# Kernel tuning notes

Hardware: AMD Instinct MI355X
Metric: run time of the kernel (lower is better)

Reference implementation:

```python
import jax, jax.numpy as jnp
import numpy as np
import math

B, S, D, H = 2, 2048, 1024, 16
HD = D // H  # head_dim = 64


def setup_inputs() -> dict:
    rng = jax.random.key(0)
    ks = jax.random.split(rng, 11)
    std = 1.0 / math.sqrt(D)
    inp = {
        "query": jax.random.normal(ks[0], (B, S, D), dtype=jnp.float32),
        "key": jax.random.normal(ks[1], (B, S, D), dtype=jnp.float32),
        "value": jax.random.normal(ks[2], (B, S, D), dtype=jnp.float32),
        # causal mask: True = masked (ignored), matching masked_fill semantics
        "mask": jnp.triu(jnp.ones((S, S), dtype=bool), k=1),
        "wq": jax.random.normal(ks[3], (D, D), dtype=jnp.float32) * std,
        "bq": jnp.zeros((D,), dtype=jnp.float32),
        "wk": jax.random.normal(ks[4], (D, D), dtype=jnp.float32) * std,
        "bk": jnp.zeros((D,), dtype=jnp.float32),
        "wv": jax.random.normal(ks[5], (D, D), dtype=jnp.float32) * std,
        "bv": jnp.zeros((D,), dtype=jnp.float32),
        "wo": jax.random.normal(ks[6], (D, D), dtype=jnp.float32) * std,
        "bo": jnp.zeros((D,), dtype=jnp.float32),
    }
    return inp


def reference(query, key, value, mask, wq, bq, wk, bk, wv, bv, wo, bo):
    # Linear projections (torch Linear: x @ W.T + b)
    q = jnp.einsum('bsd,ed->bse', query, wq) + bq
    k = jnp.einsum('bsd,ed->bse', key, wk) + bk
    v = jnp.einsum('bsd,ed->bse', value, wv) + bv
    # split heads: (B, S, D) -> (B, H, S, HD)
    q = q.reshape(B, S, H, HD).transpose(0, 2, 1, 3)
    k = k.reshape(B, S, H, HD).transpose(0, 2, 1, 3)
    v = v.reshape(B, S, H, HD).transpose(0, 2, 1, 3)
    # naive attention: materialize full (B, H, Sq, Sk) scores
    scores = jnp.einsum('bhqd,bhkd->bhqk', q, k) / jnp.sqrt(jnp.float32(HD))
    scores = jnp.where(mask[None, None, :, :], -jnp.inf, scores)
    attn = jax.nn.softmax(scores, axis=-1)
    out = jnp.einsum('bhqk,bhkd->bhqd', attn, v)
    out = out.transpose(0, 2, 1, 3).reshape(B, S, D)
    return jnp.einsum('bsd,ed->bse', out, wo) + bo
```

## Files before the change

kernel.cpp:

```cpp
#include <hip/hip_runtime.h>
#include <stdint.h>

#define B_ 2
#define S_ 2048
#define D_ 1024
#define H_ 16
#define HD_ 64
#define M_TOT (B_*S_)
#define NSPL 3

typedef __bf16 bf16;
typedef bf16 bf16x8 __attribute__((ext_vector_type(8)));
typedef float f32x4 __attribute__((ext_vector_type(4)));
typedef float f32x16 __attribute__((ext_vector_type(16)));
typedef unsigned int u32;
typedef unsigned int u32x4v __attribute__((ext_vector_type(4)));

__device__ __forceinline__ void gload_lds16(const void* g, void* l) {
    __builtin_amdgcn_global_load_lds((const __attribute__((address_space(1))) void*)g,
                                     (__attribute__((address_space(3))) void*)l, 16, 0, 0);
}

__device__ __forceinline__ u32 cvtpk_bf16(float lo, float hi) {
    u32 d;
    asm("v_cvt_pk_bf16_f32 %0, %1, %2" : "=v"(d) : "v"(lo), "v"(hi));
    return d;
}

__global__ __launch_bounds__(256) void cvt_kernel(
    const float* __restrict__ q, const float* __restrict__ k, const float* __restrict__ v,
    const float* __restrict__ wq, const float* __restrict__ wk,
    const float* __restrict__ wv, const float* __restrict__ wo,
    bf16* __restrict__ xq, bf16* __restrict__ xk, bf16* __restrict__ xv,
    bf16* __restrict__ wqb, bf16* __restrict__ wkb, bf16* __restrict__ wvb, bf16* __restrict__ wob)
{
    const float* src; bf16* dst; int n;
    switch (blockIdx.y) {
        case 0: src=q;  dst=xq;  n=M_TOT*D_; break;
        case 1: src=k;  dst=xk;  n=M_TOT*D_; break;
        case 2: src=v;  dst=xv;  n=M_TOT*D_; break;
        case 3: src=wq; dst=wqb; n=D_*D_;    break;
        case 4: src=wk; dst=wkb; n=D_*D_;    break;
        case 5: src=wv; dst=wvb; n=D_*D_;    break;
        default: src=wo; dst=wob; n=D_*D_;   break;
    }
    int i = (blockIdx.x*blockDim.x + threadIdx.x)*8;
    if (i >= n) return;
    const f32x4* s4 = (const f32x4*)(src + i);
    f32x4 a = s4[0], b = s4[1];
    bf16x8 o;
    #pragma unroll
    for (int j = 0; j < 4; ++j) { o[j] = (bf16)a[j]; o[j+4] = (bf16)b[j]; }
    *(bf16x8*)(dst + i) = o;
}

__device__ __forceinline__ void gemm_mainloop(const bf16* __restrict__ A, const bf16* __restrict__ Wt,
                                              int brow, int bcol, bf16* As, bf16* Bs,
                                              f32x4 (&acc)[4][4])
{
    const int tid = threadIdx.x;
    const int l = tid & 63, w = tid >> 6;
    const int wr = w >> 1, wc = w & 1;
    const int lr = l & 15, lq = l >> 4;

    for (int k0 = 0; k0 < D_; k0 += 32) {
        #pragma unroll
        for (int i = 0; i < 2; ++i) {
            int id = i*256 + tid;
            int row = id >> 2, c8 = (id & 3) << 3;
            gload_lds16(A  + (size_t)(brow + row)*D_ + k0 + c8, As + id*8);
            gload_lds16(Wt + (size_t)(bcol + row)*D_ + k0 + c8, Bs + id*8);
        }
        __syncthreads();
        bf16x8 af[4], bf[4];
        #pragma unroll
        for (int m = 0; m < 4; ++m)
            af[m] = *(const bf16x8*)&As[(wr*64 + m*16 + lr)*32 + lq*8];
        #pragma unroll
        for (int n = 0; n < 4; ++n)
            bf[n] = *(const bf16x8*)&Bs[(wc*64 + n*16 + lr)*32 + lq*8];
        #pragma unroll
        for (int m = 0; m < 4; ++m)
            #pragma unroll
            for (int n = 0; n < 4; ++n)
                acc[m][n] = __builtin_amdgcn_mfma_f32_16x16x32_bf16(af[m], bf[n], acc[m][n], 0, 0, 0);
        __syncthreads();
    }
}

__global__ __launch_bounds__(256) void gemm_qkv(
    const bf16* __restrict__ xq, const bf16* __restrict__ xk, const bf16* __restrict__ xv,
    const bf16* __restrict__ wqb, const bf16* __restrict__ wkb, const bf16* __restrict__ wvb,
    const float* __restrict__ bq, const float* __restrict__ bk, const float* __restrict__ bv,
    bf16* __restrict__ Qf, bf16* __restrict__ Kf, bf16* __restrict__ Vf)
{
    __shared__ __align__(16) bf16 As[128*32];
    __shared__ __align__(16) bf16 Bs[128*32];
    const int z = blockIdx.z;
    const bf16* A  = (z==0) ? xq  : (z==1) ? xk  : xv;
    const bf16* Wt = (z==0) ? wqb : (z==1) ? wkb : wvb;
    const float* bias = (z==0) ? bq : (z==1) ? bk : bv;

    const int brow = (blockIdx.x & 31)*128;
    const int bcol = (blockIdx.x >> 5)*128;

    f32x4 acc[4][4] = {};
    gemm_mainloop(A, Wt, brow, bcol, As, Bs, acc);

    const int tid = threadIdx.x;
    const int l = tid & 63, w = tid >> 6;
    const int wr = w >> 1, wc = w & 1;
    const int lr = l & 15, lq = l >> 4;

    #pragma unroll
    for (int m = 0; m < 4; ++m)
        #pragma unroll
        for (int n = 0; n < 4; ++n) {
            int col = bcol + wc*64 + n*16 + lr;
            float bv_ = bias[col];
            int h = col >> 6, hd = col & 63;
            #pragma unroll
            for (int r = 0; r < 4; ++r) {
                int row = brow + wr*64 + m*16 + lq*4 + r;
                int b = row >> 11, s = row & 2047;
                float val = acc[m][n][r] + bv_;
                if (z == 0) val *= 0.18033688011112042f;
                size_t hbase = ((size_t)b*H_ + h)*S_*HD_;
                if (z < 2) {
                    int chunk = ((s >> 5) << 2) + (hd >> 4);
                    int lane  = (((hd >> 3) & 1) << 5) | (s & 31);
                    bf16* dst = (z==0) ? Qf : Kf;
                    dst[hbase + (size_t)chunk*512 + lane*8 + (hd & 7)] = (bf16)val;
                } else {
                    int chunk = ((s >> 6) << 3) + (((s >> 4) & 3) << 1) + (hd >> 5);
                    int lane  = (((s >> 3) & 1) << 5) | (hd & 31);
                    Vf[hbase + (size_t)chunk*512 + lane*8 + (s & 7)] = (bf16)val;
                }
            }
        }
}

__global__ __launch_bounds__(256) void gemm_out(
    const bf16* __restrict__ Oat, const bf16* __restrict__ wob,
    const float* __restrict__ bo, float* __restrict__ out)
{
    __shared__ __align__(16) bf16 As[128*32];
    __shared__ __align__(16) bf16 Bs[128*32];
    const int brow = (blockIdx.x & 31)*128;
    const int bcol = (blockIdx.x >> 5)*128;

    f32x4 acc[4][4] = {};
    gemm_mainloop(Oat, wob, brow, bcol, As, Bs, acc);

    const int tid = threadIdx.x;
    const int l = tid & 63, w = tid >> 6;
    const int wr = w >> 1, wc = w & 1;
    const int lr = l & 15, lq = l >> 4;

    #pragma unroll
    for (int m = 0; m < 4; ++m)
        #pragma unroll
        for (int n = 0; n < 4; ++n) {
            int col = bcol + wc*64 + n*16 + lr;
            float bv_ = bo[col];
            #pragma unroll
            for (int r = 0; r < 4; ++r) {
                int row = brow + wr*64 + m*16 + lq*4 + r;
                out[(size_t)row*D_ + col] = acc[m][n][r] + bv_;
            }
        }
}

#define ATTN_BODY(CUR, NXT, KT) do {                                                        \
    const int kc0_ = (KT)*64;                                                               \
    const bool last_ = ((KT) == nkt - 1);                                                   \
    const int ktn_ = ((KT) + 1 < te) ? (KT) + 1 : (KT);                                     \
    bf16x8 va0[4], va1[4];                                                                  \
    _Pragma("unroll")                                                                       \
    for (int c = 0; c < 4; ++c) {                                                           \
        va0[c] = *(const bf16x8*)(Vfp + (size_t)((KT)*8 + c*2 + 0)*512 + l8);               \
        va1[c] = *(const bf16x8*)(Vfp + (size_t)((KT)*8 + c*2 + 1)*512 + l8);               \
    }                                                                                       \
    _Pragma("unroll")                                                                       \
    for (int kv2 = 0; kv2 < 2; ++kv2)                                                       \
        _Pragma("unroll")                                                                   \
        for (int dc = 0; dc < 4; ++dc)                                                      \
            NXT[kv2][dc] = *(const bf16x8*)(Kfp + (size_t)((ktn_*2 + kv2)*4 + dc)*512 + l8);\
    f32x16 ct0 = {}, ct1 = {};                                                              \
    __builtin_amdgcn_s_setprio(1);                                                          \
    _Pragma("unroll")                                                                       \
    for (int dc = 0; dc < 4; ++dc)                                                          \
        ct0 = __builtin_amdgcn_mfma_f32_32x32x16_bf16(CUR[0][dc], qb[dc], ct0, 0, 0, 0);    \
    _Pragma("unroll")                                                                       \
    for (int dc = 0; dc < 4; ++dc)                                                          \
        ct1 = __builtin_amdgcn_mfma_f32_32x32x16_bf16(CUR[1][dc], qb[dc], ct1, 0, 0, 0);    \
    __builtin_amdgcn_s_setprio(0);                                                          \
    if (last_) {                                                                            \
        _Pragma("unroll")                                                                   \
        for (int reg = 0; reg < 16; ++reg) {                                                \
            const int rr = (reg & 3) + 8*(reg >> 2) + 4*hi;                                 \
            if (kc0_ + rr > qrow)      ct0[reg] = -1e30f;                                   \
            if (kc0_ + 32 + rr > qrow) ct1[reg] = -1e30f;                                   \
        }                                                                                   \
    }                                                                                       \
    float t8[8];                                                                            \
    _Pragma("unroll")                                                                       \
    for (int i = 0; i < 8; ++i)                                                             \
        t8[i] = fmaxf(fmaxf(ct0[i], ct0[i+8]), fmaxf(ct1[i], ct1[i+8]));                    \
    float t4a = fmaxf(t8[0], t8[4]), t4b = fmaxf(t8[1], t8[5]);                             \
    float t4c = fmaxf(t8[2], t8[6]), t4d = fmaxf(t8[3], t8[7]);                             \
    float vm = fmaxf(fmaxf(t4a, t4b), fmaxf(t4c, t4d));                                     \
    vm = fmaxf(vm, __shfl_xor(vm, 32));                                                     \
    if (!__all(vm <= mrun + 8.f)) {                                                         \
        float nm = fmaxf(mrun, vm);                                                         \
        float al = exp2f(mrun - nm);                                                        \
        _Pragma("unroll")                                                                   \
        for (int i = 0; i < 16; ++i) { ot0[i] *= al; ot1[i] *= al; }                        \
        lrun *= al;                                                                         \
        mrun = nm;                                                                          \
    }                                                                                       \
    _Pragma("unroll")                                                                       \
    for (int i = 0; i < 16; ++i) {                                                          \
        ct0[i] = exp2f(ct0[i] - mrun);                                                      \
        ct1[i] = exp2f(ct1[i] - mrun);                                                      \
    }                                                                                       \
    float s8[8];                                                                            \
    _Pragma("unroll")                                                                       \
    for (int i = 0; i < 8; ++i)                                                             \
        s8[i] = (ct0[i] + ct0[i+8]) + (ct1[i] + ct1[i+8]);                                  \
    float s4a = s8[0]+s8[4], s4b = s8[1]+s8[5], s4c = s8[2]+s8[6], s4d = s8[3]+s8[7];       \
    float ps = (s4a + s4b) + (s4c + s4d);                                                   \
    ps += __shfl_xor(ps, 32);                                                               \
    lrun += ps;                                                                             \
    u32 own0[8], own1[8], oth0[8], oth1[8];                                                 \
    _Pragma("unroll")                                                                       \
    for (int u = 0; u < 8; ++u) {                                                           \
        own0[u] = cvtpk_bf16(ct0[2*u], ct0[2*u+1]);                                         \
        own1[u] = cvtpk_bf16(ct1[2*u], ct1[2*u+1]);                                         \
    }                                                                                       \
    _Pragma("unroll")                                                                       \
    for (int u = 0; u < 8; ++u) {                                                           \
        oth0[u] = __shfl_xor(own0[u], 32);                                                  \
        oth1[u] = __shfl_xor(own1[u], 32);                                                  \
    }                                                                                       \
    __builtin_amdgcn_s_setprio(1);                                                          \
    _Pragma("unroll")                                                                       \
    for (int c = 0; c < 4; ++c) {                                                           \
        const int b0 = 4*(c & 1);                                                           \
        u32 o0, o1, o2, o3, x0, x1, x2, x3;                                                 \
        if ((c >> 1) == 0) {                                                                \
            o0 = own0[b0]; o1 = own0[b0+1]; o2 = own0[b0+2]; o3 = own0[b0+3];               \
            x0 = oth0[b0]; x1 = oth0[b0+1]; x2 = oth0[b0+2]; x3 = oth0[b0+3];               \
        } else {                                                                            \
            o0 = own1[b0]; o1 = own1[b0+1]; o2 = own1[b0+2]; o3 = own1[b0+3];               \
            x0 = oth1[b0]; x1 = oth1[b0+1]; x2 = oth1[b0+2]; x3 = oth1[b0+3];               \
        }                                                                                   \
        u32 w0 = hi ? x2 : o0;                                                              \
        u32 w1 = hi ? x3 : o1;                                                              \
        u32 w2 = hi ? o2 : x0;                                                              \
        u32 w3 = hi ? o3 : x1;                                                              \
        u32x4v pw = { w0, w1, w2, w3 };                                                     \
        bf16x8 pb = __builtin_bit_cast(bf16x8, pw);                                         \
        ot0 = __builtin_amdgcn_mfma_f32_32x32x16_bf16(va0[c], pb, ot0, 0, 0, 0);            \
        ot1 = __builtin_amdgcn_mfma_f32_32x32x16_bf16(va1[c], pb, ot1, 0, 0, 0);            \
    }                                                                                       \
    __builtin_amdgcn_s_setprio(0);                                                          \
} while (0)

__global__ __launch_bounds__(64, 2) void attn_part(
    const bf16* __restrict__ Qf, const bf16* __restrict__ Kf,
    const bf16* __restrict__ Vf, bf16* __restrict__ Opart, float* __restrict__ Mlf)
{
    const int l = threadIdx.x & 63;
    const int l31 = l & 31, hi = l >> 5;
    const int l8 = l*8;

    const int id = (int)blockIdx.x;
    const int xcd = id & 7;
    const int slot = id >> 3;
    const int bh = xcd + 8*(slot/192);
    const int rem = slot % 192;
    const int qt = 63 - rem/3;
    const int part = rem % 3;
    const int q0 = qt*32;
    const int qrow = q0 + l31;
    const int widx = (bh*64 + qt)*NSPL + part;

    const bf16* Qfp = Qf + (size_t)bh*S_*HD_;
    const bf16* Kfp = Kf + (size_t)bh*S_*HD_;
    const bf16* Vfp = Vf + (size_t)bh*S_*HD_;

    const int nkt = q0/64 + 1;
    const int ts = (part*nkt)/NSPL;
    const int te = ((part+1)*nkt)/NSPL;

    bf16x8 qb[4];
    #pragma unroll
    for (int dc = 0; dc < 4; ++dc)
        qb[dc] = *(const bf16x8*)(Qfp + (size_t)(((q0 >> 5) << 2) + dc)*512 + l8);

    f32x16 ot0 = {}, ot1 = {};
    float mrun = -1e30f, lrun = 0.f;

    if (ts < te) {
        bf16x8 ka[2][4], kb[2][4];
        #pragma unroll
        for (int kv2 = 0; kv2 < 2; ++kv2)
            #pragma unroll
            for (int dc = 0; dc < 4; ++dc)
                ka[kv2][dc] = *(const bf16x8*)(Kfp + (size_t)((ts*2 + kv2)*4 + dc)*512 + l8);

        int kt = ts;
        while (kt + 1 < te) {
            ATTN_BODY(ka, kb, kt); ++kt;
            ATTN_BODY(kb, ka, kt); ++kt;
        }
        if (kt < te) {
            ATTN_BODY(ka, kb, kt);
        }
    }

    bf16* Ob = Opart + (size_t)widx*2048;
    #pragma unroll
    for (int rp = 0; rp < 16; ++rp) {
        const int d0 = (rp & 3) + 8*(rp >> 2) + 4*hi;
        Ob[d0*32 + l31]        = (bf16)ot0[rp];
        Ob[(32 + d0)*32 + l31] = (bf16)ot1[rp];
    }
    if (!hi) {
        Mlf[(size_t)widx*64 + l31*2]     = mrun;
        Mlf[(size_t)widx*64 + l31*2 + 1] = lrun;
    }
}

__global__ __launch_bounds__(64) void attn_combine(
    const bf16* __restrict__ Opart, const float* __restrict__ Mlf, bf16* __restrict__ Oat)
{
    const int cb = (int)blockIdx.x;
    const int bh = cb >> 6, qt = cb & 63;
    const int b = bh >> 4, h = bh & 15;
    const int q0 = qt*32;
    const int l = threadIdx.x & 63;
    const int q = l & 31, hi = l >> 5;

    const int wbase = (bh*64 + qt)*NSPL;
    float mm[NSPL], ll[NSPL];
    #pragma unroll
    for (int p = 0; p < NSPL; ++p) {
        mm[p] = Mlf[(size_t)(wbase+p)*64 + q*2];
        ll[p] = Mlf[(size_t)(wbase+p)*64 + q*2 + 1];
    }
    float m = fmaxf(fmaxf(mm[0], mm[1]), mm[2]);
    float f[NSPL];
    float lt = 0.f;
    #pragma unroll
    for (int p = 0; p < NSPL; ++p) { f[p] = exp2f(mm[p] - m); lt += ll[p]*f[p]; }
    const float inv = 1.f / lt;
    #pragma unroll
    for (int p = 0; p < NSPL; ++p) f[p] *= inv;

    char* rowp = (char*)Oat + (((size_t)(b*S_ + q0 + q)*D_ + h*64 + hi*32)*2);

    #pragma unroll
    for (int i = 0; i < 16; ++i) {
        const int d = hi*32 + 2*i;
        float oA = 0.f, oB = 0.f;
        #pragma unroll
        for (int p = 0; p < NSPL; ++p) {
            const bf16* Op = Opart + (size_t)(wbase+p)*2048;
            oA += (float)Op[d*32 + q]*f[p];
            oB += (float)Op[(d+1)*32 + q]*f[p];
        }
        *(u32*)(rowp + 4*i) = cvtpk_bf16(oA, oB);
    }
}

extern "C" void kernel_launch(void* const* d_in, const int* in_sizes, int n_in,
                              void* d_out, int out_size, void* d_ws, size_t ws_size,
                              hipStream_t stream) {
    const float* q  = (const float*)d_in[0];
    const float* k  = (const float*)d_in[1];
    const float* v  = (const float*)d_in[2];
    const float* wq = (const float*)d_in[4];
    const float* bq = (const float*)d_in[5];
    const float* wk = (const float*)d_in[6];
    const float* bk = (const float*)d_in[7];
    const float* wv = (const float*)d_in[8];
    const float* bv = (const float*)d_in[9];
    const float* wo = (const float*)d_in[10];
    const float* bo = (const float*)d_in[11];
    float* out = (float*)d_out;

    char* p = (char*)d_ws;
    const size_t XSZ = (size_t)M_TOT*D_*sizeof(bf16);
    const size_t WSZ = (size_t)D_*D_*sizeof(bf16);
    bf16* xq  = (bf16*)p;
    bf16* xk  = (bf16*)(p + XSZ);
    bf16* xv  = (bf16*)(p + 2*XSZ);
    bf16* wqb = (bf16*)(p + 3*XSZ);
    bf16* wkb = (bf16*)(p + 3*XSZ + WSZ);
    bf16* wvb = (bf16*)(p + 3*XSZ + 2*WSZ);
    bf16* wob = (bf16*)(p + 3*XSZ + 3*WSZ);
    bf16* Qf  = (bf16*)(p + 3*XSZ + 4*WSZ);
    bf16* Kf  = Qf + M_TOT*D_;
    bf16* Vf  = Kf + M_TOT*D_;
    bf16* Oat = Vf + M_TOT*D_;
    bf16*  Opart = (bf16*)p;
    float* Mlf   = (float*)(p + 3*XSZ);

    cvt_kernel<<<dim3(2048, 7), 256, 0, stream>>>(q, k, v, wq, wk, wv, wo,
                                                  xq, xk, xv, wqb, wkb, wvb, wob);
    gemm_qkv<<<dim3(256, 1, 3), 256, 0, stream>>>(xq, xk, xv, wqb, wkb, wvb,
                                                  bq, bk, bv, Qf, Kf, Vf);
    attn_part<<<32*64*NSPL, 64, 0, stream>>>(Qf, Kf, Vf, Opart, Mlf);
    attn_combine<<<2048, 64, 0, stream>>>(Opart, Mlf, Oat);
    gemm_out<<<dim3(256), 256, 0, stream>>>(Oat, wob, bo, out);
}
```

Measured before the change: 130.4 us.

## Fuse fp32-to-bf16 conversion into GEMM LDS loads and drop conversion kernel

Removes the separate conversion kernel and has the QKV and output GEMMs load fp32 inputs and weights directly into LDS with an XOR swizzle, converting to bf16 when fragments are read. This avoids a full extra read/write pass over activations and weights plus one launch. In exchange, GEMM tiles move twice the bytes through global memory and LDS, and every fragment read repeats the conversion, raising shared memory use and possibly lowering occupancy.

```diff
diff --git a/kernel.cpp b/kernel.cpp
--- a/kernel.cpp
+++ b/kernel.cpp
@@ -27,36 +27,18 @@
     return d;
 }
 
-__global__ __launch_bounds__(256) void cvt_kernel(
-    const float* __restrict__ q, const float* __restrict__ k, const float* __restrict__ v,
-    const float* __restrict__ wq, const float* __restrict__ wk,
-    const float* __restrict__ wv, const float* __restrict__ wo,
-    bf16* __restrict__ xq, bf16* __restrict__ xk, bf16* __restrict__ xv,
-    bf16* __restrict__ wqb, bf16* __restrict__ wkb, bf16* __restrict__ wvb, bf16* __restrict__ wob)
-{
-    const float* src; bf16* dst; int n;
-    switch (blockIdx.y) {
-        case 0: src=q;  dst=xq;  n=M_TOT*D_; break;
-        case 1: src=k;  dst=xk;  n=M_TOT*D_; break;
-        case 2: src=v;  dst=xv;  n=M_TOT*D_; break;
-        case 3: src=wq; dst=wqb; n=D_*D_;    break;
-        case 4: src=wk; dst=wkb; n=D_*D_;    break;
-        case 5: src=wv; dst=wvb; n=D_*D_;    break;
-        default: src=wo; dst=wob; n=D_*D_;   break;
-    }
-    int i = (blockIdx.x*blockDim.x + threadIdx.x)*8;
-    if (i >= n) return;
-    const f32x4* s4 = (const f32x4*)(src + i);
-    f32x4 a = s4[0], b = s4[1];
-    bf16x8 o;
-    #pragma unroll
-    for (int j = 0; j < 4; ++j) { o[j] = (bf16)a[j]; o[j+4] = (bf16)b[j]; }
-    *(bf16x8*)(dst + i) = o;
-}
-
-__device__ __forceinline__ void gemm_mainloop(const bf16* __restrict__ A, const bf16* __restrict__ Wt,
-                                              int brow, int bcol, bf16* As, bf16* Bs,
-                                              f32x4 (&acc)[4][4])
+__device__ __forceinline__ bf16x8 cvt8(f32x4 a, f32x4 b) {
+    u32x4v r;
+    r[0] = cvtpk_bf16(a[0], a[1]);
+    r[1] = cvtpk_bf16(a[2], a[3]);
+    r[2] = cvtpk_bf16(b[0], b[1]);
+    r[3] = cvtpk_bf16(b[2], b[3]);
+    return __builtin_bit_cast(bf16x8, r);
+}
+
+__device__ __forceinline__ void gemm_mainloop_f32(const float* __restrict__ A, const float* __restrict__ Wt,
+                                                  int brow, int bcol, float* As, float* Bs,
+                                                  f32x4 (&acc)[4][4])
 {
     const int tid = threadIdx.x;
     const int l = tid & 63, w = tid >> 6;
@@ -65,20 +47,29 @@
 
     for (int k0 = 0; k0 < D_; k0 += 32) {
         #pragma unroll
-        for (int i = 0; i < 2; ++i) {
+        for (int i = 0; i < 4; ++i) {
             int id = i*256 + tid;
-            int row = id >> 2, c8 = (id & 3) << 3;
-            gload_lds16(A  + (size_t)(brow + row)*D_ + k0 + c8, As + id*8);
-            gload_lds16(Wt + (size_t)(bcol + row)*D_ + k0 + c8, Bs + id*8);
+            int row = id >> 3, c16 = id & 7;
+            int sc = (c16 ^ (row & 7)) << 2;
+            gload_lds16(A  + (size_t)(brow + row)*D_ + k0 + sc, (char*)As + id*16);
+            gload_lds16(Wt + (size_t)(bcol + row)*D_ + k0 + sc, (char*)Bs + id*16);
         }
         __syncthreads();
         bf16x8 af[4], bf[4];
         #pragma unroll
-        for (int m = 0; m < 4; ++m)
-            af[m] = *(const bf16x8*)&As[(wr*64 + m*16 + lr)*32 + lq*8];
-        #pragma unroll
-        for (int n = 0; n < 4; ++n)
-            bf[n] = *(const bf16x8*)&Bs[(wc*64 + n*16 + lr)*32 + lq*8];
+        for (int m = 0; m < 4; ++m) {
+            int row = wr*64 + m*16 + lr, r7 = row & 7;
+            f32x4 a0 = *(const f32x4*)(As + row*32 + (((lq*2    ) ^ r7) << 2));
+            f32x4 a1 = *(const f32x4*)(As + row*32 + (((lq*2 + 1) ^ r7) << 2));
+            af[m] = cvt8(a0, a1);
+        }
+        #pragma unroll
+        for (int n = 0; n < 4; ++n) {
+            int row = wc*64 + n*16 + lr, r7 = row & 7;
+            f32x4 b0 = *(const f32x4*)(Bs + row*32 + (((lq*2    ) ^ r7) << 2));
+            f32x4 b1 = *(const f32x4*)(Bs + row*32 + (((lq*2 + 1) ^ r7) << 2));
+            bf[n] = cvt8(b0, b1);
+        }
         #pragma unroll
         for (int m = 0; m < 4; ++m)
             #pragma unroll
@@ -89,23 +80,23 @@
 }
 
 __global__ __launch_bounds__(256) void gemm_qkv(
-    const bf16* __restrict__ xq, const bf16* __restrict__ xk, const bf16* __restrict__ xv,
-    const bf16* __restrict__ wqb, const bf16* __restrict__ wkb, const bf16* __restrict__ wvb,
+    const float* __restrict__ xq, const float* __restrict__ xk, const float* __restrict__ xv,
+    const float* __restrict__ wqf, const float* __restrict__ wkf, const float* __restrict__ wvf,
     const float* __restrict__ bq, const float* __restrict__ bk, const float* __restrict__ bv,
     bf16* __restrict__ Qf, bf16* __restrict__ Kf, bf16* __restrict__ Vf)
 {
-    __shared__ __align__(16) bf16 As[128*32];
-    __shared__ __align__(16) bf16 Bs[128*32];
+    __shared__ __align__(16) float As[128*32];
+    __shared__ __align__(16) float Bs[128*32];
     const int z = blockIdx.z;
-    const bf16* A  = (z==0) ? xq  : (z==1) ? xk  : xv;
-    const bf16* Wt = (z==0) ? wqb : (z==1) ? wkb : wvb;
+    const float* A  = (z==0) ? xq  : (z==1) ? xk  : xv;
+    const float* Wt = (z==0) ? wqf : (z==1) ? wkf : wvf;
     const float* bias = (z==0) ? bq : (z==1) ? bk : bv;
 
     const int brow = (blockIdx.x & 31)*128;
     const int bcol = (blockIdx.x >> 5)*128;
 
     f32x4 acc[4][4] = {};
-    gemm_mainloop(A, Wt, brow, bcol, As, Bs, acc);
+    gemm_mainloop_f32(A, Wt, brow, bcol, As, Bs, acc);
 
     const int tid = threadIdx.x;
     const int l = tid & 63, w = tid >> 6;
@@ -141,21 +132,54 @@
 }
 
 __global__ __launch_bounds__(256) void gemm_out(
-    const bf16* __restrict__ Oat, const bf16* __restrict__ wob,
+    const bf16* __restrict__ Oat, const float* __restrict__ wof,
     const float* __restrict__ bo, float* __restrict__ out)
 {
-    __shared__ __align__(16) bf16 As[128*32];
-    __shared__ __align__(16) bf16 Bs[128*32];
+    __shared__ __align__(16) bf16  As[128*32];
+    __shared__ __align__(16) float Bs[128*32];
     const int brow = (blockIdx.x & 31)*128;
     const int bcol = (blockIdx.x >> 5)*128;
-
-    f32x4 acc[4][4] = {};
-    gemm_mainloop(Oat, wob, brow, bcol, As, Bs, acc);
 
     const int tid = threadIdx.x;
     const int l = tid & 63, w = tid >> 6;
     const int wr = w >> 1, wc = w & 1;
     const int lr = l & 15, lq = l >> 4;
+
+    f32x4 acc[4][4] = {};
+
+    for (int k0 = 0; k0 < D_; k0 += 32) {
+        #pragma unroll
+        for (int i = 0; i < 2; ++i) {
+            int id = i*256 + tid;
+            int row = id >> 2, c8 = (id & 3) << 3;
+            gload_lds16(Oat + (size_t)(brow + row)*D_ + k0 + c8, (char*)As + id*16);
+        }
+        #pragma unroll
+        for (int i = 0; i < 4; ++i) {
+            int id = i*256 + tid;
+            int row = id >> 3, c16 = id & 7;
+            int sc = (c16 ^ (row & 7)) << 2;
+            gload_lds16(wof + (size_t)(bcol + row)*D_ + k0 + sc, (char*)Bs + id*16);
+        }
+        __syncthreads();
+        bf16x8 af[4], bf[4];
+        #pragma unroll
+        for (int m = 0; m < 4; ++m)
+            af[m] = *(const bf16x8*)&As[(wr*64 + m*16 + lr)*32 + lq*8];
+        #pragma unroll
+        for (int n = 0; n < 4; ++n) {
+            int row = wc*64 + n*16 + lr, r7 = row & 7;
+            f32x4 b0 = *(const f32x4*)(Bs + row*32 + (((lq*2    ) ^ r7) << 2));
+            f32x4 b1 = *(const f32x4*)(Bs + row*32 + (((lq*2 + 1) ^ r7) << 2));
+            bf[n] = cvt8(b0, b1);
+        }
+        #pragma unroll
+        for (int m = 0; m < 4; ++m)
+            #pragma unroll
+            for (int n = 0; n < 4; ++n)
+                acc[m][n] = __builtin_amdgcn_mfma_f32_16x16x32_bf16(af[m], bf[n], acc[m][n], 0, 0, 0);
+        __syncthreads();
+    }
 
     #pragma unroll
     for (int m = 0; m < 4; ++m)
@@ -393,26 +417,16 @@
 
     char* p = (char*)d_ws;
     const size_t XSZ = (size_t)M_TOT*D_*sizeof(bf16);
-    const size_t WSZ = (size_t)D_*D_*sizeof(bf16);
-    bf16* xq  = (bf16*)p;
-    bf16* xk  = (bf16*)(p + XSZ);
-    bf16* xv  = (bf16*)(p + 2*XSZ);
-    bf16* wqb = (bf16*)(p + 3*XSZ);
-    bf16* wkb = (bf16*)(p + 3*XSZ + WSZ);
-    bf16* wvb = (bf16*)(p + 3*XSZ + 2*WSZ);
-    bf16* wob = (bf16*)(p + 3*XSZ + 3*WSZ);
-    bf16* Qf  = (bf16*)(p + 3*XSZ + 4*WSZ);
+    bf16*  Opart = (bf16*)p;
+    float* Mlf   = (float*)(p + 3*XSZ);
+    bf16* Qf  = (bf16*)(p + 4*XSZ);
     bf16* Kf  = Qf + M_TOT*D_;
     bf16* Vf  = Kf + M_TOT*D_;
     bf16* Oat = Vf + M_TOT*D_;
-    bf16*  Opart = (bf16*)p;
-    float* Mlf   = (float*)(p + 3*XSZ);
-
-    cvt_kernel<<<dim3(2048, 7), 256, 0, stream>>>(q, k, v, wq, wk, wv, wo,
-                                                  xq, xk, xv, wqb, wkb, wvb, wob);
-    gemm_qkv<<<dim3(256, 1, 3), 256, 0, stream>>>(xq, xk, xv, wqb, wkb, wvb,
+
+    gemm_qkv<<<dim3(256, 1, 3), 256, 0, stream>>>(q, k, v, wq, wk, wv,
                                                   bq, bk, bv, Qf, Kf, Vf);
     attn_part<<<32*64*NSPL, 64, 0, stream>>>(Qf, Kf, Vf, Opart, Mlf);
     attn_combine<<<2048, 64, 0, stream>>>(Opart, Mlf, Oat);
-    gemm_out<<<dim3(256), 256, 0, stream>>>(Oat, wob, bo, out);
-}
+    gemm_out<<<dim3(256), 256, 0, stream>>>(Oat, wo, bo, out);
+}
```

Result: slower. 143.6 us (+10.1%).
